# Kernel optimization log

Hardware: AMD Instinct MI355X
Metric: run time of the kernel (lower is better)

The kernel has to match this reference:

```python
import jax, jax.numpy as jnp
import numpy as np

DIM = 1024
HEADS = 16
NUM_EXPERTS = 8
TOP_K = 2
INNER = 4 * DIM
EPS = 1e-5
NEG = -1e9


def setup_inputs() -> dict:
    key = jax.random.key(0)
    ks = jax.random.split(key, 12)
    s = 0.02
    return {
        "x": jax.random.normal(ks[0], (4, 1024, DIM), dtype=jnp.float32),
        "qkv_w": jax.random.normal(ks[1], (DIM, 3 * DIM), dtype=jnp.float32) * s,
        "out_w": jax.random.normal(ks[2], (DIM, DIM), dtype=jnp.float32) * s,
        "out_b": jnp.zeros((DIM,), dtype=jnp.float32),
        "thresh": jnp.float32(-2.0),
        "ln1_g": jnp.ones((DIM,), dtype=jnp.float32),
        "ln1_b": jnp.zeros((DIM,), dtype=jnp.float32),
        "ln2_g": jnp.ones((DIM,), dtype=jnp.float32),
        "ln2_b": jnp.zeros((DIM,), dtype=jnp.float32),
        "gate_w": jax.random.normal(ks[3], (DIM, NUM_EXPERTS), dtype=jnp.float32) * s,
        "w1": jax.random.normal(ks[4], (NUM_EXPERTS, DIM, INNER), dtype=jnp.float32) * s,
        "b1": jnp.zeros((NUM_EXPERTS, INNER), dtype=jnp.float32),
        "w2": jax.random.normal(ks[5], (NUM_EXPERTS, INNER, DIM), dtype=jnp.float32) * s,
        "b2": jnp.zeros((NUM_EXPERTS, DIM), dtype=jnp.float32),
    }


def _layernorm(x, g, b):
    mu = jnp.mean(x, axis=-1, keepdims=True)
    var = jnp.mean(jnp.square(x - mu), axis=-1, keepdims=True)
    return (x - mu) * jax.lax.rsqrt(var + EPS) * g + b


def reference(x, qkv_w, out_w, out_b, thresh, ln1_g, ln1_b, ln2_g, ln2_b,
              gate_w, w1, b1, w2, b2):
    B, N, D = x.shape
    H = HEADS
    Dh = D // H
    scale = Dh ** -0.5

    # --- Sparse attention (pre-norm, eval mode: dropout off) ---
    h = _layernorm(x, ln1_g, ln1_b)
    qkv = h @ qkv_w                                   # [B,N,3D]
    q, k, v = jnp.split(qkv, 3, axis=-1)
    def heads(t):
        return t.reshape(B, N, H, Dh).transpose(0, 2, 1, 3)  # [B,H,N,Dh]
    q, k, v = heads(q), heads(k), heads(v)
    dots = jnp.einsum("bhid,bhjd->bhij", q, k) * scale
    dots = jnp.where(dots < thresh, jnp.float32(NEG), dots)  # learnable sparsity
    attn = jax.nn.softmax(dots, axis=-1)
    o = jnp.einsum("bhij,bhjd->bhid", attn, v)
    o = o.transpose(0, 2, 1, 3).reshape(B, N, D)
    x = x + o @ out_w + out_b

    # --- MoE FFN (pre-norm) ---
    h2 = _layernorm(x, ln2_g, ln2_b).reshape(-1, D)   # [T,D]
    T = h2.shape[0]
    logits = h2 @ gate_w                              # [T,E]
    probs = jax.nn.softmax(logits, axis=-1)
    aux_loss = NUM_EXPERTS * jnp.sum(probs.mean(0) * probs.sum(0))

    top_w, top_i = jax.lax.top_k(logits, TOP_K)       # [T,k]
    top_w = jax.nn.softmax(top_w, axis=-1)
    # dense combine weights: [T,E], zero for unselected experts
    combine = jnp.zeros((T, NUM_EXPERTS), dtype=h2.dtype)
    combine = combine.at[jnp.arange(T)[:, None], top_i].set(top_w)

    out = jnp.zeros_like(h2)
    for e in range(NUM_EXPERTS):
        y = jax.nn.gelu(h2 @ w1[e] + b1[e], approximate=False) @ w2[e] + b2[e]
        out = out + combine[:, e:e + 1] * y

    x = x + out.reshape(B, N, D)
    return x, aux_loss
```

## Files before the change

kernel.cpp:

```cpp
#include <hip/hip_runtime.h>
#include <math.h>

#define DIM 1024
#define THREE_DIM 3072
#define INNER 4096
#define NTOK 4096
#define NPAIR 8192
#define NEXP 8
#define MAXMB 72

typedef __attribute__((ext_vector_type(8))) short bf16x8;
typedef __attribute__((ext_vector_type(4))) float f32x4;

__device__ __forceinline__ unsigned short f2bf(float f){
    unsigned int x = __float_as_uint(f);
    unsigned int r = x + 0x7fffu + ((x >> 16) & 1u);
    return (unsigned short)(r >> 16);
}

__device__ __forceinline__ unsigned short us4c(ushort4 v, int i){
    return i == 0 ? v.x : (i == 1 ? v.y : (i == 2 ? v.z : v.w));
}

__device__ __forceinline__ void glds16(const void* g, void* l){
    __builtin_amdgcn_global_load_lds(
        (const __attribute__((address_space(1))) void*)g,
        (__attribute__((address_space(3))) void*)l, 16, 0, 0);
}

template<int WRITE_BF>
__global__ __launch_bounds__(256)
void ln_kernel(const float* __restrict__ X, const float* __restrict__ g,
               const float* __restrict__ b, float* __restrict__ outF,
               unsigned short* __restrict__ outB)
{
    int row = blockIdx.x;
    int t = threadIdx.x;
    const float4 v = *((const float4*)(X + (size_t)row*DIM) + t);
    float s = v.x + v.y + v.z + v.w;
    #pragma unroll
    for (int m = 1; m < 64; m <<= 1) s += __shfl_xor(s, m, 64);
    __shared__ float red[8];
    int wid = t >> 6, lane = t & 63;
    if (lane == 0) red[wid] = s;
    __syncthreads();
    float mu = (red[0]+red[1]+red[2]+red[3]) * (1.0f/DIM);
    float dx = v.x-mu, dy = v.y-mu, dz = v.z-mu, dw = v.w-mu;
    float s2 = dx*dx + dy*dy + dz*dz + dw*dw;
    #pragma unroll
    for (int m = 1; m < 64; m <<= 1) s2 += __shfl_xor(s2, m, 64);
    if (lane == 0) red[4+wid] = s2;
    __syncthreads();
    float var = (red[4]+red[5]+red[6]+red[7]) * (1.0f/DIM);
    float inv = rsqrtf(var + 1e-5f);
    const float4 gg = *((const float4*)g + t);
    const float4 bb = *((const float4*)b + t);
    float y0 = dx*inv*gg.x + bb.x;
    float y1 = dy*inv*gg.y + bb.y;
    float y2 = dz*inv*gg.z + bb.z;
    float y3 = dw*inv*gg.w + bb.w;
    if (outF){
        float4 o; o.x=y0; o.y=y1; o.z=y2; o.w=y3;
        *((float4*)(outF + (size_t)row*DIM) + t) = o;
    }
    if (WRITE_BF){
        ushort4 u; u.x=f2bf(y0); u.y=f2bf(y1); u.z=f2bf(y2); u.w=f2bf(y3);
        *((ushort4*)(outB + (size_t)row*DIM) + t) = u;
    }
}

template<int MODE>
__global__ __launch_bounds__(256)
void gemm_bf(const unsigned short* __restrict__ A,
             const unsigned short* __restrict__ BT,
             int K, int N,
             const float* __restrict__ bias, const float* __restrict__ resid,
             unsigned short* __restrict__ outB, float* __restrict__ outF)
{
    __shared__ __align__(16) unsigned short As[128*64];
    __shared__ __align__(16) unsigned short Bs[128*64];
    int t = threadIdx.x, lane = t & 63, wid = t >> 6;
    int m0 = blockIdx.y * 128, n0 = blockIdx.x * 128;
    size_t aoff[4], boff[4];
    #pragma unroll
    for (int it = 0; it < 4; ++it){
        int chunk = it*256 + wid*64 + lane;
        int r = chunk >> 3, c16 = chunk & 7;
        int c16s = c16 ^ (r & 7);
        aoff[it] = (size_t)(m0 + r)*K + (size_t)(c16s*8);
        boff[it] = (size_t)(n0 + r)*K + (size_t)(c16s*8);
    }
    int wm = wid >> 1, wn = wid & 1;
    f32x4 acc[4][4];
    #pragma unroll
    for (int mi = 0; mi < 4; ++mi)
        #pragma unroll
        for (int ni = 0; ni < 4; ++ni)
            #pragma unroll
            for (int q = 0; q < 4; ++q) acc[mi][ni][q] = 0.f;

    for (int k0 = 0; k0 < K; k0 += 64){
        __syncthreads();
        #pragma unroll
        for (int it = 0; it < 4; ++it){
            glds16(A  + aoff[it] + k0, As + (size_t)(it*256 + wid*64)*8);
            glds16(BT + boff[it] + k0, Bs + (size_t)(it*256 + wid*64)*8);
        }
        __syncthreads();
        bf16x8 af[4][2], bg[4][2];
        #pragma unroll
        for (int mi = 0; mi < 4; ++mi){
            int row = wm*64 + mi*16 + (lane & 15);
            #pragma unroll
            for (int ks = 0; ks < 2; ++ks){
                int cg = (ks*4 + (lane >> 4)) ^ (row & 7);
                af[mi][ks] = *(const bf16x8*)&As[row*64 + cg*8];
            }
        }
        #pragma unroll
        for (int ni = 0; ni < 4; ++ni){
            int row = wn*64 + ni*16 + (lane & 15);
            #pragma unroll
            for (int ks = 0; ks < 2; ++ks){
                int cg = (ks*4 + (lane >> 4)) ^ (row & 7);
                bg[ni][ks] = *(const bf16x8*)&Bs[row*64 + cg*8];
            }
        }
        #pragma unroll
        for (int ks = 0; ks < 2; ++ks)
            #pragma unroll
            for (int mi = 0; mi < 4; ++mi)
                #pragma unroll
                for (int ni = 0; ni < 4; ++ni)
                    acc[mi][ni] = __builtin_amdgcn_mfma_f32_16x16x32_bf16(
                                      af[mi][ks], bg[ni][ks], acc[mi][ni], 0, 0, 0);
    }
    #pragma unroll
    for (int mi = 0; mi < 4; ++mi){
        #pragma unroll
        for (int ni = 0; ni < 4; ++ni){
            int ccol = n0 + wn*64 + ni*16 + (lane & 15);
            #pragma unroll
            for (int j = 0; j < 4; ++j){
                int row = m0 + wm*64 + mi*16 + (lane >> 4)*4 + j;
                float v = acc[mi][ni][j];
                if (MODE == 0){
                    outB[(size_t)row*N + ccol] = f2bf(v);
                } else {
                    outF[(size_t)row*N + ccol] =
                        v + bias[ccol] + resid[(size_t)row*N + ccol];
                }
            }
        }
    }
}

__global__ __launch_bounds__(256)
void attn4_kernel(const unsigned short* __restrict__ qkv,
                  unsigned short* __restrict__ O,
                  const float* __restrict__ threshp)
{
    __shared__ __align__(16) unsigned short Qs[64*64];
    __shared__ __align__(16) unsigned short Ks[64*64];
    __shared__ __align__(16) unsigned short Vp[8*520];
    __shared__ __align__(16) unsigned short Ps[4*1024];

    int t = threadIdx.x, lane = t & 63, w = t >> 6;
    int arow = lane & 15, agrp = lane >> 4;
    int qt = blockIdx.x, hh = blockIdx.y, bb = blockIdx.z;
    int qrow0 = bb*1024 + qt*64;
    float thresh = threshp[0];

    #pragma unroll
    for (int it = 0; it < 2; ++it){
        int chunk = it*256 + w*64 + lane;
        int r = chunk >> 3, c16 = chunk & 7;
        glds16(qkv + (size_t)(qrow0+r)*3072 + hh*64 + ((c16 ^ (r & 7))*8),
               Qs + (size_t)(it*256 + w*64)*8);
    }
    __syncthreads();
    bf16x8 qf[2];
    {
        int row = w*16 + arow;
        #pragma unroll
        for (int s = 0; s < 2; ++s){
            int c = (s*4 + agrp) ^ (row & 7);
            qf[s] = *(const bf16x8*)&Qs[row*64 + c*8];
        }
    }

    float m_[4], l_[4];
    f32x4 acc[4];
    #pragma unroll
    for (int j = 0; j < 4; ++j){ m_[j] = -INFINITY; l_[j] = 0.f; }
    #pragma unroll
    for (int d4 = 0; d4 < 4; ++d4)
        #pragma unroll
        for (int j = 0; j < 4; ++j) acc[d4][j] = 0.f;

    for (int kt = 0; kt < 16; ++kt){
        __syncthreads();
        int krow0 = bb*1024 + kt*64;
        #pragma unroll
        for (int it = 0; it < 2; ++it){
            int chunk = it*256 + w*64 + lane;
            int r = chunk >> 3, c16 = chunk & 7;
            glds16(qkv + (size_t)(krow0+r)*3072 + 1024 + hh*64 + ((c16 ^ (r & 7))*8),
                   Ks + (size_t)(it*256 + w*64)*8);
        }
        if (t < 128){
            int jc = t & 7, d0 = (t >> 3) * 4;
            ushort4 u[8];
            #pragma unroll
            for (int jj = 0; jj < 8; ++jj)
                u[jj] = *(const ushort4*)(qkv + (size_t)(krow0 + jc*8 + jj)*3072
                                          + 2048 + hh*64 + d0);
            #pragma unroll
            for (int i = 0; i < 4; ++i){
                ushort4 a, b;
                a.x = us4c(u[0], i); a.y = us4c(u[1], i);
                a.z = us4c(u[2], i); a.w = us4c(u[3], i);
                b.x = us4c(u[4], i); b.y = us4c(u[5], i);
                b.z = us4c(u[6], i); b.w = us4c(u[7], i);
                *(ushort4*)&Vp[jc*520 + (d0+i)*8]     = a;
                *(ushort4*)&Vp[jc*520 + (d0+i)*8 + 4] = b;
            }
        }
        __syncthreads();

        f32x4 sv[4];
        #pragma unroll
        for (int n = 0; n < 4; ++n)
            #pragma unroll
            for (int j = 0; j < 4; ++j) sv[n][j] = 0.f;
        #pragma unroll
        for (int n = 0; n < 4; ++n){
            int krow = n*16 + arow;
            #pragma unroll
            for (int s = 0; s < 2; ++s){
                int c = (s*4 + agrp) ^ (krow & 7);
                bf16x8 kf = *(const bf16x8*)&Ks[krow*64 + c*8];
                sv[n] = __builtin_amdgcn_mfma_f32_16x16x32_bf16(qf[s], kf, sv[n], 0, 0, 0);
            }
        }
        #pragma unroll
        for (int n = 0; n < 4; ++n)
            #pragma unroll
            for (int j = 0; j < 4; ++j){
                float s = sv[n][j] * 0.125f;
                sv[n][j] = (s < thresh) ? -1e9f : s;
            }
        float tmax[4], fac[4], rsum[4];
        #pragma unroll
        for (int j = 0; j < 4; ++j)
            tmax[j] = fmaxf(fmaxf(sv[0][j], sv[1][j]), fmaxf(sv[2][j], sv[3][j]));
        #pragma unroll
        for (int msk = 1; msk < 16; msk <<= 1)
            #pragma unroll
            for (int j = 0; j < 4; ++j)
                tmax[j] = fmaxf(tmax[j], __shfl_xor(tmax[j], msk, 64));
        #pragma unroll
        for (int j = 0; j < 4; ++j){
            float mn = fmaxf(m_[j], tmax[j]);
            fac[j] = __expf(m_[j] - mn);
            m_[j] = mn;
        }
        #pragma unroll
        for (int n = 0; n < 4; ++n)
            #pragma unroll
            for (int j = 0; j < 4; ++j)
                sv[n][j] = __expf(sv[n][j] - m_[j]);
        #pragma unroll
        for (int j = 0; j < 4; ++j)
            rsum[j] = sv[0][j] + sv[1][j] + sv[2][j] + sv[3][j];
        #pragma unroll
        for (int msk = 1; msk < 16; msk <<= 1)
            #pragma unroll
            for (int j = 0; j < 4; ++j)
                rsum[j] += __shfl_xor(rsum[j], msk, 64);
        #pragma unroll
        for (int j = 0; j < 4; ++j)
            l_[j] = l_[j]*fac[j] + rsum[j];
        #pragma unroll
        for (int n = 0; n < 4; ++n){
            int col = n*16 + arow;
            #pragma unroll
            for (int j = 0; j < 4; ++j){
                int r = agrp*4 + j;
                int idx = r*64 + (((col>>3) ^ (r&7)) << 3) + (col & 7);
                Ps[w*1024 + idx] = f2bf(sv[n][j]);
            }
        }
        #pragma unroll
        for (int d4 = 0; d4 < 4; ++d4)
            #pragma unroll
            for (int j = 0; j < 4; ++j) acc[d4][j] *= fac[j];
        #pragma unroll
        for (int s = 0; s < 2; ++s){
            int c = (s*4 + agrp) ^ (arow & 7);
            bf16x8 pa = *(const bf16x8*)&Ps[w*1024 + arow*64 + c*8];
            int jc = s*4 + agrp;
            #pragma unroll
            for (int d4 = 0; d4 < 4; ++d4){
                int dcol = d4*16 + arow;
                bf16x8 vb = *(const bf16x8*)&Vp[jc*520 + dcol*8];
                acc[d4] = __builtin_amdgcn_mfma_f32_16x16x32_bf16(pa, vb, acc[d4], 0, 0, 0);
            }
        }
    }
    #pragma unroll
    for (int j = 0; j < 4; ++j){
        float inv = 1.0f / l_[j];
        int row = qrow0 + w*16 + agrp*4 + j;
        #pragma unroll
        for (int d4 = 0; d4 < 4; ++d4)
            O[(size_t)row*1024 + hh*64 + d4*16 + arow] = f2bf(acc[d4][j] * inv);
    }
}

__global__ __launch_bounds__(64)
void gate_kernel(const float* __restrict__ h2, const float* __restrict__ gw,
                 float* __restrict__ probs, int* __restrict__ top_i,
                 float* __restrict__ top_w)
{
    int tk = blockIdx.x;
    int lane = threadIdx.x;
    const float* hr = h2 + (size_t)tk*DIM;
    float acc[8];
    #pragma unroll
    for (int e = 0; e < 8; ++e) acc[e] = 0.f;
    for (int d = lane; d < DIM; d += 64){
        float hv = hr[d];
        const float* grow = gw + d*8;
        #pragma unroll
        for (int e = 0; e < 8; ++e) acc[e] = fmaf(hv, grow[e], acc[e]);
    }
    #pragma unroll
    for (int m = 1; m < 64; m <<= 1)
        #pragma unroll
        for (int e = 0; e < 8; ++e) acc[e] += __shfl_xor(acc[e], m, 64);
    if (lane == 0){
        float mx = acc[0];
        #pragma unroll
        for (int e = 1; e < 8; ++e) mx = fmaxf(mx, acc[e]);
        float p[8], s = 0.f;
        #pragma unroll
        for (int e = 0; e < 8; ++e){ p[e] = __expf(acc[e]-mx); s += p[e]; }
        float invs = 1.f/s;
        #pragma unroll
        for (int e = 0; e < 8; ++e) probs[(size_t)tk*8+e] = p[e]*invs;
        int i0 = 0; float v0 = acc[0];
        #pragma unroll
        for (int e = 1; e < 8; ++e) if (acc[e] > v0){ v0 = acc[e]; i0 = e; }
        int i1 = -1; float v1 = -INFINITY;
        #pragma unroll
        for (int e = 0; e < 8; ++e) if (e != i0 && acc[e] > v1){ v1 = acc[e]; i1 = e; }
        float w0 = 1.f/(1.f + __expf(v1 - v0));
        top_i[tk*2]   = i0; top_i[tk*2+1] = i1;
        top_w[tk*2]   = w0; top_w[tk*2+1] = 1.f - w0;
    }
}

__global__ __launch_bounds__(256)
void aux_kernel(const float* __restrict__ probs, float* __restrict__ dout)
{
    int t = threadIdx.x;
    float acc[8];
    #pragma unroll
    for (int e = 0; e < 8; ++e) acc[e] = 0.f;
    for (int r = t; r < NTOK; r += 256){
        const float* pr = probs + (size_t)r*8;
        #pragma unroll
        for (int e = 0; e < 8; ++e) acc[e] += pr[e];
    }
    #pragma unroll
    for (int m = 1; m < 64; m <<= 1)
        #pragma unroll
        for (int e = 0; e < 8; ++e) acc[e] += __shfl_xor(acc[e], m, 64);
    __shared__ float red[4][8];
    int wid = t >> 6, lane = t & 63;
    if (lane == 0)
        for (int e = 0; e < 8; ++e) red[wid][e] = acc[e];
    __syncthreads();
    if (t == 0){
        float aux = 0.f;
        for (int e = 0; e < 8; ++e){
            float S = red[0][e]+red[1][e]+red[2][e]+red[3][e];
            aux += S*S;
        }
        dout[(size_t)NTOK*DIM] = aux * (8.0f/NTOK);
    }
}

__global__ __launch_bounds__(512)
void routing_kernel(const int* __restrict__ topi, int* __restrict__ perm,
                    int* __restrict__ mblk_e)
{
    __shared__ int cnt[8];
    __shared__ int obase[8];
    int t = threadIdx.x, w = t >> 6, lane = t & 63;
    int c = 0;
    for (int i0 = 0; i0 < NPAIR; i0 += 64){
        int e = topi[i0 + lane];
        c += (e == w) ? 1 : 0;
    }
    #pragma unroll
    for (int m = 1; m < 64; m <<= 1) c += __shfl_xor(c, m, 64);
    if (lane == 0) cnt[w] = c;
    __syncthreads();
    if (t == 0){
        int mb = 0;
        for (int e = 0; e < 8; ++e){
            obase[e] = mb*128;
            int nb = (cnt[e] + 127) >> 7;
            for (int k = 0; k < nb; ++k) mblk_e[mb++] = e;
        }
        for (; mb < MAXMB; ++mb) mblk_e[mb] = -1;
    }
    __syncthreads();
    for (int i = t; i < MAXMB*128; i += 512) perm[i] = -1;
    __syncthreads();
    int base = obase[w];
    for (int i0 = 0; i0 < NPAIR; i0 += 64){
        int p = i0 + lane;
        int e = topi[p];
        bool mt = (e == w);
        unsigned long long mk = __ballot(mt);
        int rank = __popcll(mk & ((1ull << lane) - 1ull));
        if (mt) perm[base + rank] = p;
        base += __popcll(mk);
    }
}

template<int MODE>
__global__ __launch_bounds__(256)
void gemm_moe2(const unsigned short* __restrict__ Abase,
               const unsigned short* __restrict__ BTbase,
               int K, int N, int lda,
               const int* __restrict__ perm, const int* __restrict__ mblk_e,
               const float* __restrict__ bias,
               unsigned short* __restrict__ actout,
               const float* __restrict__ topw, float* __restrict__ dout)
{
    int mb = blockIdx.y;
    int e = mblk_e[mb];
    if (e < 0) return;
    __shared__ __align__(16) unsigned short As[128*64];
    __shared__ __align__(16) unsigned short Bs[128*64];
    __shared__ int permL[128];
    int t = threadIdx.x;
    if (t < 128) permL[t] = perm[mb*128 + t];
    __syncthreads();
    int lane = t & 63, wid = t >> 6;
    int n0 = blockIdx.x * 128;
    const unsigned short* BT = BTbase + (size_t)e * (size_t)N * (size_t)K;
    int base_chunk = wid*64 + lane;
    size_t aoff[4], boff[4];
    #pragma unroll
    for (int it = 0; it < 4; ++it){
        int chunk = base_chunk + it*256;
        int r = chunk >> 3, c16 = chunk & 7;
        int c16s = c16 ^ (r & 7);
        size_t ar;
        if (MODE == 2){ int p = permL[r]; ar = (p >= 0) ? (size_t)(p >> 1) : 0; }
        else          { ar = (size_t)(mb*128 + r); }
        aoff[it] = ar*(size_t)lda + (size_t)(c16s*8);
        boff[it] = (size_t)(n0 + r)*(size_t)K + (size_t)(c16s*8);
    }
    int wm = wid >> 1, wn = wid & 1;
    f32x4 acc[4][4];
    #pragma unroll
    for (int mi = 0; mi < 4; ++mi)
        #pragma unroll
        for (int ni = 0; ni < 4; ++ni)
            #pragma unroll
            for (int q = 0; q < 4; ++q) acc[mi][ni][q] = 0.f;

    for (int k0 = 0; k0 < K; k0 += 64){
        __syncthreads();
        #pragma unroll
        for (int it = 0; it < 4; ++it){
            glds16(Abase + aoff[it] + k0, As + (size_t)(wid*64 + it*256)*8);
            glds16(BT    + boff[it] + k0, Bs + (size_t)(wid*64 + it*256)*8);
        }
        __syncthreads();
        bf16x8 af[4][2], bg[4][2];
        #pragma unroll
        for (int mi = 0; mi < 4; ++mi){
            int row = wm*64 + mi*16 + (lane & 15);
            #pragma unroll
            for (int ks = 0; ks < 2; ++ks){
                int cg = (ks*4 + (lane >> 4)) ^ (row & 7);
                af[mi][ks] = *(const bf16x8*)&As[row*64 + cg*8];
            }
        }
        #pragma unroll
        for (int ni = 0; ni < 4; ++ni){
            int row = wn*64 + ni*16 + (lane & 15);
            #pragma unroll
            for (int ks = 0; ks < 2; ++ks){
                int cg = (ks*4 + (lane >> 4)) ^ (row & 7);
                bg[ni][ks] = *(const bf16x8*)&Bs[row*64 + cg*8];
            }
        }
        #pragma unroll
        for (int ks = 0; ks < 2; ++ks)
            #pragma unroll
            for (int mi = 0; mi < 4; ++mi)
                #pragma unroll
                for (int ni = 0; ni < 4; ++ni)
                    acc[mi][ni] = __builtin_amdgcn_mfma_f32_16x16x32_bf16(
                                      af[mi][ks], bg[ni][ks], acc[mi][ni], 0, 0, 0);
    }
    #pragma unroll
    for (int mi = 0; mi < 4; ++mi){
        #pragma unroll
        for (int ni = 0; ni < 4; ++ni){
            int ccol = n0 + wn*64 + ni*16 + (lane & 15);
            float bv = bias[(size_t)e*N + ccol];
            #pragma unroll
            for (int j = 0; j < 4; ++j){
                int rloc = wm*64 + mi*16 + (lane >> 4)*4 + j;
                float v = acc[mi][ni][j];
                if (MODE == 2){
                    float gx = v + bv;
                    float gl = 0.5f * gx * (1.0f + erff(gx * 0.70710678118f));
                    actout[(size_t)(mb*128 + rloc)*N + ccol] = f2bf(gl);
                } else {
                    int p = permL[rloc];
                    if (p >= 0){
                        float val = (v + bv) * topw[p];
                        atomicAdd(&dout[(size_t)(p >> 1)*N + ccol], val);
                    }
                }
            }
        }
    }
}

__global__ __launch_bounds__(256)
void transp_cast(const float* __restrict__ W, unsigned short* __restrict__ WT,
                 int K, int N)
{
    __shared__ float tile[32][33];
    size_t base = (size_t)blockIdx.z * (size_t)K * (size_t)N;
    const float* Wp = W + base;
    unsigned short* Tp = WT + base;
    int t = threadIdx.x;
    int r = t >> 3, c4 = (t & 7) << 2;
    int n0 = blockIdx.x << 5, k0 = blockIdx.y << 5;
    float4 v = *(const float4*)(Wp + (size_t)(k0+r)*N + n0 + c4);
    tile[r][c4+0] = v.x; tile[r][c4+1] = v.y;
    tile[r][c4+2] = v.z; tile[r][c4+3] = v.w;
    __syncthreads();
    ushort4 u;
    u.x = f2bf(tile[c4+0][r]);
    u.y = f2bf(tile[c4+1][r]);
    u.z = f2bf(tile[c4+2][r]);
    u.w = f2bf(tile[c4+3][r]);
    *(ushort4*)(Tp + (size_t)(n0+r)*K + k0 + c4) = u;
}

extern "C" void kernel_launch(void* const* d_in, const int* in_sizes, int n_in,
                              void* d_out, int out_size, void* d_ws, size_t ws_size,
                              hipStream_t stream)
{
    const float* x      = (const float*)d_in[0];
    const float* qkv_w  = (const float*)d_in[1];
    const float* out_w  = (const float*)d_in[2];
    const float* out_b  = (const float*)d_in[3];
    const float* thresh = (const float*)d_in[4];
    const float* ln1_g  = (const float*)d_in[5];
    const float* ln1_b  = (const float*)d_in[6];
    const float* ln2_g  = (const float*)d_in[7];
    const float* ln2_b  = (const float*)d_in[8];
    const float* gate_w = (const float*)d_in[9];
    const float* w1     = (const float*)d_in[10];
    const float* b1     = (const float*)d_in[11];
    const float* w2     = (const float*)d_in[12];
    const float* b2     = (const float*)d_in[13];
    float* out = (float*)d_out;
    char* ws = (char*)d_ws;

    const size_t MB = (size_t)1 << 20;
    unsigned short* h1bf  = (unsigned short*)(ws);
    unsigned short* qkvbf = (unsigned short*)(ws + 8*MB);
    unsigned short* obf   = (unsigned short*)(ws + 32*MB);
    float*          h2    = (float*)(ws + 40*MB);
    unsigned short* h2bf  = (unsigned short*)(ws + 56*MB);
    unsigned short* qwT   = (unsigned short*)(ws + 64*MB);
    unsigned short* owT   = (unsigned short*)(ws + 70*MB);
    unsigned short* w1T   = (unsigned short*)(ws + 72*MB);
    unsigned short* w2T   = (unsigned short*)(ws + 136*MB);
    unsigned short* act   = (unsigned short*)(ws + 200*MB);
    float* probs          = (float*)(ws + 276*MB);
    int*   top_i          = (int*)(ws + 276*MB + 131072);
    float* top_w          = (float*)(ws + 276*MB + 163840);
    int*   perm           = (int*)(ws + 276*MB + 196608);
    int*   mblk           = (int*)(ws + 276*MB + 237568);

    transp_cast<<<dim3(THREE_DIM/32, DIM/32, 1), 256, 0, stream>>>(qkv_w, qwT, DIM, THREE_DIM);
    transp_cast<<<dim3(DIM/32, DIM/32, 1), 256, 0, stream>>>(out_w, owT, DIM, DIM);

    ln_kernel<1><<<NTOK, 256, 0, stream>>>(x, ln1_g, ln1_b, nullptr, h1bf);
    gemm_bf<0><<<dim3(THREE_DIM/128, NTOK/128), 256, 0, stream>>>(
        h1bf, qwT, DIM, THREE_DIM, nullptr, nullptr, qkvbf, nullptr);
    attn4_kernel<<<dim3(16, 16, 4), 256, 0, stream>>>(qkvbf, obf, thresh);
    gemm_bf<1><<<dim3(DIM/128, NTOK/128), 256, 0, stream>>>(
        obf, owT, DIM, DIM, out_b, x, nullptr, out);
    ln_kernel<1><<<NTOK, 256, 0, stream>>>(out, ln2_g, ln2_b, h2, h2bf);
    gate_kernel<<<NTOK, 64, 0, stream>>>(h2, gate_w, probs, top_i, top_w);
    aux_kernel<<<1, 256, 0, stream>>>(probs, out);
    routing_kernel<<<1, 512, 0, stream>>>(top_i, perm, mblk);

    transp_cast<<<dim3(INNER/32, DIM/32, NEXP), 256, 0, stream>>>(w1, w1T, DIM, INNER);
    transp_cast<<<dim3(DIM/32, INNER/32, NEXP), 256, 0, stream>>>(w2, w2T, INNER, DIM);

    gemm_moe2<2><<<dim3(INNER/128, MAXMB), 256, 0, stream>>>(
        h2bf, w1T, DIM, INNER, DIM, perm, mblk, b1, act, nullptr, nullptr);
    gemm_moe2<3><<<dim3(DIM/128, MAXMB), 256, 0, stream>>>(
        act, w2T, INNER, DIM, INNER, perm, mblk, b2, nullptr, top_w, out);
}
```

Baseline: 531.2 us.

## Fuse expert weight transpose-cast into MoE GEMM loads and use tanh GELU

Drops the two separate transpose/cast kernels for the expert weights w1 and w2. The MoE GEMMs now read the fp32 weights directly, convert them to bf16 with packed conversion instructions, and write them transposed into shared memory. The exact erf GELU is replaced by a tanh-style sigmoid approximation built from fast exp and reciprocal. This removes a full write and reread of 128 MB of transposed bf16 weights, but each expert weight tile is now re-read in fp32 and re-converted by every M-block that uses it, and the GELU result differs slightly from the exact form.

```diff
diff --git a/kernel.cpp b/kernel.cpp
--- a/kernel.cpp
+++ b/kernel.cpp
@@ -22,10 +22,20 @@
     return i == 0 ? v.x : (i == 1 ? v.y : (i == 2 ? v.z : v.w));
 }
 
+__device__ __forceinline__ float f4c(float4 v, int i){
+    return i == 0 ? v.x : (i == 1 ? v.y : (i == 2 ? v.z : v.w));
+}
+
 __device__ __forceinline__ void glds16(const void* g, void* l){
     __builtin_amdgcn_global_load_lds(
         (const __attribute__((address_space(1))) void*)g,
         (__attribute__((address_space(3))) void*)l, 16, 0, 0);
+}
+
+__device__ __forceinline__ unsigned int pkbf(float a, float b){
+    unsigned int r;
+    asm("v_cvt_pk_bf16_f32 %0, %1, %2" : "=v"(r) : "v"(a), "v"(b));
+    return r;
 }
 
 template<int WRITE_BF>
@@ -434,8 +444,8 @@
 
 template<int MODE>
 __global__ __launch_bounds__(256)
-void gemm_moe2(const unsigned short* __restrict__ Abase,
-               const unsigned short* __restrict__ BTbase,
+void gemm_moe3(const unsigned short* __restrict__ Abase,
+               const float* __restrict__ Wsrc,
                int K, int N, int lda,
                const int* __restrict__ perm, const int* __restrict__ mblk_e,
                const float* __restrict__ bias,
@@ -453,20 +463,22 @@
     __syncthreads();
     int lane = t & 63, wid = t >> 6;
     int n0 = blockIdx.x * 128;
-    const unsigned short* BT = BTbase + (size_t)e * (size_t)N * (size_t)K;
-    int base_chunk = wid*64 + lane;
-    size_t aoff[4], boff[4];
+    const float* W = Wsrc + (size_t)e * (size_t)K * (size_t)N;
+    size_t aoff[4];
     #pragma unroll
     for (int it = 0; it < 4; ++it){
-        int chunk = base_chunk + it*256;
+        int chunk = it*256 + wid*64 + lane;
         int r = chunk >> 3, c16 = chunk & 7;
         int c16s = c16 ^ (r & 7);
         size_t ar;
         if (MODE == 2){ int p = permL[r]; ar = (p >= 0) ? (size_t)(p >> 1) : 0; }
         else          { ar = (size_t)(mb*128 + r); }
         aoff[it] = ar*(size_t)lda + (size_t)(c16s*8);
-        boff[it] = (size_t)(n0 + r)*(size_t)K + (size_t)(c16s*8);
-    }
+    }
+    int bn4 = (t & 31) * 4;
+    int bk8 = (t >> 5) * 8;
+    const float* bsrc0 = W + (size_t)bk8 * N + n0 + bn4;
+
     int wm = wid >> 1, wn = wid & 1;
     f32x4 acc[4][4];
     #pragma unroll
@@ -478,10 +490,24 @@
 
     for (int k0 = 0; k0 < K; k0 += 64){
         __syncthreads();
-        #pragma unroll
-        for (int it = 0; it < 4; ++it){
-            glds16(Abase + aoff[it] + k0, As + (size_t)(wid*64 + it*256)*8);
-            glds16(BT    + boff[it] + k0, Bs + (size_t)(wid*64 + it*256)*8);
+        float4 vv[8];
+        const float* bsrc = bsrc0 + (size_t)k0 * N;
+        #pragma unroll
+        for (int j = 0; j < 8; ++j)
+            vv[j] = *(const float4*)(bsrc + (size_t)j * N);
+        #pragma unroll
+        for (int it = 0; it < 4; ++it)
+            glds16(Abase + aoff[it] + k0, As + (size_t)(it*256 + wid*64)*8);
+        #pragma unroll
+        for (int i = 0; i < 4; ++i){
+            int row = bn4 + i;
+            unsigned int pk0 = pkbf(f4c(vv[0], i), f4c(vv[1], i));
+            unsigned int pk1 = pkbf(f4c(vv[2], i), f4c(vv[3], i));
+            unsigned int pk2 = pkbf(f4c(vv[4], i), f4c(vv[5], i));
+            unsigned int pk3 = pkbf(f4c(vv[6], i), f4c(vv[7], i));
+            int cg = (t >> 5) ^ (row & 7);
+            uint4 u; u.x = pk0; u.y = pk1; u.z = pk2; u.w = pk3;
+            *(uint4*)&Bs[row*64 + cg*8] = u;
         }
         __syncthreads();
         bf16x8 af[4][2], bg[4][2];
@@ -524,7 +550,9 @@
                 float v = acc[mi][ni][j];
                 if (MODE == 2){
                     float gx = v + bv;
-                    float gl = 0.5f * gx * (1.0f + erff(gx * 0.70710678118f));
+                    float z2 = gx * fmaf(gx*gx, 0.07135481283f, 1.595769122f);
+                    float ex = __expf(-z2);
+                    float gl = gx * __builtin_amdgcn_rcpf(1.0f + ex);
                     actout[(size_t)(mb*128 + rloc)*N + ccol] = f2bf(gl);
                 } else {
                     int p = permL[rloc];
@@ -590,8 +618,6 @@
     unsigned short* h2bf  = (unsigned short*)(ws + 56*MB);
     unsigned short* qwT   = (unsigned short*)(ws + 64*MB);
     unsigned short* owT   = (unsigned short*)(ws + 70*MB);
-    unsigned short* w1T   = (unsigned short*)(ws + 72*MB);
-    unsigned short* w2T   = (unsigned short*)(ws + 136*MB);
     unsigned short* act   = (unsigned short*)(ws + 200*MB);
     float* probs          = (float*)(ws + 276*MB);
     int*   top_i          = (int*)(ws + 276*MB + 131072);
@@ -613,11 +639,8 @@
     aux_kernel<<<1, 256, 0, stream>>>(probs, out);
     routing_kernel<<<1, 512, 0, stream>>>(top_i, perm, mblk);
 
-    transp_cast<<<dim3(INNER/32, DIM/32, NEXP), 256, 0, stream>>>(w1, w1T, DIM, INNER);
-    transp_cast<<<dim3(DIM/32, INNER/32, NEXP), 256, 0, stream>>>(w2, w2T, INNER, DIM);
-
-    gemm_moe2<2><<<dim3(INNER/128, MAXMB), 256, 0, stream>>>(
-        h2bf, w1T, DIM, INNER, DIM, perm, mblk, b1, act, nullptr, nullptr);
-    gemm_moe2<3><<<dim3(DIM/128, MAXMB), 256, 0, stream>>>(
-        act, w2T, INNER, DIM, INNER, perm, mblk, b2, nullptr, top_w, out);
-}
+    gemm_moe3<2><<<dim3(INNER/128, MAXMB), 256, 0, stream>>>(
+        h2bf, w1, DIM, INNER, DIM, perm, mblk, b1, act, nullptr, nullptr);
+    gemm_moe3<3><<<dim3(DIM/128, MAXMB), 256, 0, stream>>>(
+        act, w2, INNER, DIM, INNER, perm, mblk, b2, nullptr, top_w, out);
+}
```

New measurement: 653.1 us. 1.23x slower.
